# Performance work log

Measured on AMD Instinct MI355X. Metric: run time of the kernel, lower is better.

The kernel has to match this reference:

```python
import jax, jax.numpy as jnp
import numpy as np

B, T, C, H = 2, 2048, 1024, 16
D = C // H  # head dim, even
NEG = -1e10  # masked_fill value used by the torch module (not -inf)


def _rope_cache(dim, max_positions):
    # Faithful to source: theta_i = 1/10000**(-2*(i-1)/dim), i = arange(dim//2)
    i = jnp.arange(dim // 2, dtype=jnp.float32)
    theta = 1.0 / (10000.0 ** (-2.0 * (i - 1.0) / dim))
    ang = jnp.arange(max_positions, dtype=jnp.float32)[:, None] * theta[None, :]  # [T, D/2]
    return jnp.cos(ang), jnp.sin(ang)


def _apply_rope(x, cos, sin):
    # x: [B,H,T,D]; consecutive pairs form complex numbers (x[...,2j], x[...,2j+1])
    xp = x.reshape(*x.shape[:-1], D // 2, 2)
    xr, xi = xp[..., 0], xp[..., 1]
    rr = xr * cos - xi * sin
    ri = xr * sin + xi * cos
    return jnp.stack([rr, ri], axis=-1).reshape(x.shape)


def setup_inputs() -> dict:
    key = jax.random.key(0)
    ks = jax.random.split(key, 5)
    s = 1.0 / np.sqrt(C)
    return {
        'x': jax.random.normal(ks[0], (B, T, C), jnp.float32),
        'Wq': jax.random.normal(ks[1], (C, C), jnp.float32) * s,
        'bq': jnp.zeros((C,), jnp.float32),
        'Wk': jax.random.normal(ks[2], (C, C), jnp.float32) * s,
        'bk': jnp.zeros((C,), jnp.float32),
        'Wv': jax.random.normal(ks[3], (C, C), jnp.float32) * s,
        'bv': jnp.zeros((C,), jnp.float32),
        'Wp': jax.random.normal(ks[4], (C, C), jnp.float32) * s,
        'bp': jnp.zeros((C,), jnp.float32),
    }


def reference(x, Wq, bq, Wk, bk, Wv, bv, Wp, bp):
    cos, sin = _rope_cache(D, T)  # [T, D/2]
    def split_heads(h):
        return h.reshape(B, T, H, D).transpose(0, 2, 1, 3)  # [B,H,T,D]
    q = split_heads(x @ Wq.T + bq)
    k = split_heads(x @ Wk.T + bk)
    v = split_heads(x @ Wv.T + bv)
    q = _apply_rope(q, cos, sin)
    k = _apply_rope(k, cos, sin)
    att = jnp.einsum('bhqd,bhkd->bhqk', q, k) * (1.0 / np.sqrt(D))  # [B,H,T,T]
    causal = jnp.tril(jnp.ones((T, T), bool))
    att = jnp.where(causal, att, NEG)
    att = jax.nn.softmax(att, axis=-1)
    y = jnp.einsum('bhqk,bhkd->bhqd', att, v)
    y = y.transpose(0, 2, 1, 3).reshape(B, T, C)
    return y @ Wp.T + bp
```

## Files before the change

### kernel.cpp

```cpp
#include <hip/hip_runtime.h>

#define SEQ 2048
#define CDIM 1024
#define NHEAD 16
#define HDIM 64

typedef __bf16 bf16x8 __attribute__((ext_vector_type(8)));
typedef __bf16 bf16x4v __attribute__((ext_vector_type(4)));
typedef float f32x4 __attribute__((ext_vector_type(4)));

typedef const __attribute__((address_space(1))) char* gcp_t;
typedef __attribute__((address_space(3))) char* lcp_t;

__device__ __forceinline__ void gload16(const void* g, void* l) {
    __builtin_amdgcn_global_load_lds((gcp_t)g, (lcp_t)l, 16, 0, 0);
}

__device__ __forceinline__ unsigned short f2bf(float f) {
    unsigned int u = __float_as_uint(f);
    u += 0x7fffu + ((u >> 16) & 1u);
    return (unsigned short)(u >> 16);
}

__device__ __forceinline__ int swz16(int r) { return ((r >> 1) & 3) << 4; }


__global__ void cvt_all(const float* __restrict__ x,
                        const float* __restrict__ Wq, const float* __restrict__ Wk,
                        const float* __restrict__ Wv, const float* __restrict__ Wp,
                        unsigned short* __restrict__ xb,
                        unsigned short* __restrict__ wqkv, unsigned short* __restrict__ wpb) {
    int i = blockIdx.x * blockDim.x + threadIdx.x;
    const float* s;
    unsigned short* d;
    int r;
    if (i < 1048576) { s = x; d = xb; r = i; }
    else {
        int j = i - 1048576;
        int which = j >> 18; r = j & 262143;
        s = (which == 0) ? Wq : (which == 1) ? Wk : (which == 2) ? Wv : Wp;
        d = (which < 3) ? (wqkv + (size_t)which * 1048576) : wpb;
    }
    float4 v = ((const float4*)s)[r];
    ushort4 o;
    o.x = f2bf(v.x); o.y = f2bf(v.y); o.z = f2bf(v.z); o.w = f2bf(v.w);
    ((ushort4*)d)[r] = o;
}

__global__ void rope_kernel(float2* __restrict__ cstab) {
    int idx = blockIdx.x * blockDim.x + threadIdx.x;
    int j = idx & 31, t = idx >> 5;
    float e = -2.0f * ((float)j - 1.0f) / 64.0f;
    float denom = (float)pow(10000.0, (double)e);
    float theta = 1.0f / denom;
    float ang = (float)t * theta;
    cstab[idx] = make_float2(cosf(ang), sinf(ang));
}

__global__ __launch_bounds__(512, 1) void gemm_qkv(
    const unsigned short* __restrict__ A, const unsigned short* __restrict__ Bm,
    const float* __restrict__ b0, const float* __restrict__ b1, const float* __restrict__ b2,
    unsigned short* __restrict__ qb, unsigned short* __restrict__ kb,
    unsigned short* __restrict__ vtb, const float2* __restrict__ cstab)
{
    constexpr int NT = 16;
    __shared__ __align__(16) char As[2][256 * 128];
    __shared__ __align__(16) char Bs2[2][192 * 128];
    const int tid = threadIdx.x, lane = tid & 63, wid = tid >> 6;
    const int wr = wid >> 2, wc = wid & 3;
    const int bid = blockIdx.x;
    const int swz = (bid & 7) * 32 + (bid >> 3);
    const int mt = swz >> 4, ntl = swz & 15;
    const int m0 = mt * 256, n0 = ntl * 192;

    f32x4 acc[8][3] = {};

    const char* Ag = (const char*)A + (size_t)m0 * 2048;
    const char* Bg = (const char*)Bm + (size_t)n0 * 2048;
    const int r0 = tid >> 3, cb = (tid & 7) * 16;

    auto stage = [&](int k0, int bufi) {
#pragma unroll
        for (int v = 0; v < 4; ++v) {
            const int r = r0 + 64 * v;
            gload16(Ag + (size_t)r * 2048 + k0 * 2 + (cb ^ ((r & 7) << 4)),
                    As[bufi] + v * 8192 + wid * 1024);
        }
#pragma unroll
        for (int v = 0; v < 3; ++v) {
            const int r = r0 + 64 * v;
            gload16(Bg + (size_t)r * 2048 + k0 * 2 + (cb ^ ((r & 7) << 4)),
                    Bs2[bufi] + v * 8192 + wid * 1024);
        }
    };

    stage(0, 0);
    asm volatile("s_waitcnt vmcnt(0)" ::: "memory");
    __builtin_amdgcn_s_barrier();

    for (int t = 0; t < NT; ++t) {
        const int cur = t & 1;
        if (t + 1 < NT) stage((t + 1) * 64, cur ^ 1);
        const char* Ac = As[cur];
        const char* Bc = Bs2[cur];
#pragma unroll
        for (int kf = 0; kf < 2; ++kf) {
            bf16x8 bfr[3];
#pragma unroll
            for (int fc = 0; fc < 3; ++fc) {
                const int r = wc * 48 + fc * 16 + (lane & 15);
                bfr[fc] = *(const bf16x8*)(Bc + r * 128 + ((kf * 64 + (lane >> 4) * 16) ^ ((r & 7) << 4)));
            }
            __builtin_amdgcn_s_setprio(1);
#pragma unroll
            for (int fr = 0; fr < 8; ++fr) {
                const int r = wr * 128 + fr * 16 + (lane & 15);
                bf16x8 af = *(const bf16x8*)(Ac + r * 128 + ((kf * 64 + (lane >> 4) * 16) ^ ((r & 7) << 4)));
#pragma unroll
                for (int fc = 0; fc < 3; ++fc)
                    acc[fr][fc] = __builtin_amdgcn_mfma_f32_16x16x32_bf16(af, bfr[fc], acc[fr][fc], 0, 0, 0);
            }
            __builtin_amdgcn_s_setprio(0);
        }
        asm volatile("s_waitcnt vmcnt(0)" ::: "memory");
        __builtin_amdgcn_s_barrier();
    }

    const float QSCL = 0.18033688011112042f;
#pragma unroll
    for (int fc = 0; fc < 3; ++fc) {
        const int ng = n0 + wc * 48 + fc * 16 + (lane & 15);
        const int which = ng >> 10, nl = ng & 1023;
        const int h = nl >> 6, d = nl & 63;
        const float* bptr = (which == 0) ? b0 : (which == 1) ? b1 : b2;
        const float bias = bptr[nl];
        if (which < 2) {
            unsigned short* dst = (which == 0) ? qb : kb;
            const float qs = (which == 0) ? QSCL : 1.0f;
            const int j = d >> 1;
#pragma unroll
            for (int fr = 0; fr < 8; ++fr) {
#pragma unroll
                for (int i = 0; i < 4; ++i) {
                    const int row = m0 + wr * 128 + fr * 16 + (lane >> 4) * 4 + i;
                    const int bb = row >> 11, tt = row & 2047;
                    float v = acc[fr][fc][i] + bias;
                    float pp = __shfl_xor(v, 1);
                    const float2 cs = cstab[tt * 32 + j];
                    v = (d & 1) ? fmaf(v, cs.x, pp * cs.y) : fmaf(v, cs.x, -pp * cs.y);
                    dst[((size_t)((bb * 16 + h) * 2048 + tt)) * 64 + d] = f2bf(v * qs);
                }
            }
        } else {
#pragma unroll
            for (int fr = 0; fr < 8; ++fr) {
                const int rowb = m0 + wr * 128 + fr * 16 + (lane >> 4) * 4;
                const int bb = rowb >> 11, tt = rowb & 2047;
                ushort4 pk;
                pk.x = f2bf(acc[fr][fc][0] + bias);
                pk.y = f2bf(acc[fr][fc][1] + bias);
                pk.z = f2bf(acc[fr][fc][2] + bias);
                pk.w = f2bf(acc[fr][fc][3] + bias);
                *(ushort4*)(vtb + ((size_t)((bb * 16 + h) * 64 + d)) * 2048 + tt) = pk;
            }
        }
    }
}

template <int MODE, int BM>
__global__ __launch_bounds__(256) void gemm_bt(
    const unsigned short* __restrict__ A, const unsigned short* __restrict__ Bm,
    const float* __restrict__ b0,
    float* __restrict__ outf)
{
    constexpr int K = 1024;
    constexpr int NIT = K / 32;
    constexpr int NR = (BM == 128) ? 4 : 2;
    __shared__ __align__(16) char As[2][BM * 64];
    __shared__ __align__(16) char Bs[2][128 * 64];
    const int tid = threadIdx.x, lane = tid & 63, wid = tid >> 6;
    const int m0 = blockIdx.y * BM, n0 = blockIdx.x * 128;
    const int wr = (BM == 128) ? ((wid >> 1) * 64) : 0;
    const int wc = (BM == 128) ? ((wid & 1) * 64) : (wid * 32);

    f32x4 acc[4][NR] = {};

    const char* Ag = (const char*)(A + (size_t)m0 * K);
    const char* Bg = (const char*)(Bm + (size_t)n0 * K);
    const int r0 = tid >> 2, cb = (tid & 3) * 16;
    const int ldsw = wid << 10;

    auto stage = [&](int k0, int bufi) {
        char* Ad = As[bufi];
        char* Bd = Bs[bufi];
        gload16(Ag + (size_t)r0 * 2048 + k0 * 2 + (cb ^ swz16(r0)), Ad + ldsw);
        if constexpr (BM == 128)
            gload16(Ag + (size_t)(r0 + 64) * 2048 + k0 * 2 + (cb ^ swz16(r0 + 64)), Ad + 4096 + ldsw);
        gload16(Bg + (size_t)r0 * 2048 + k0 * 2 + (cb ^ swz16(r0)), Bd + ldsw);
        gload16(Bg + (size_t)(r0 + 64) * 2048 + k0 * 2 + (cb ^ swz16(r0 + 64)), Bd + 4096 + ldsw);
    };

    stage(0, 0);
    __syncthreads();

    for (int it = 0; it < NIT; ++it) {
        const int cur = it & 1;
        if (it + 1 < NIT) stage((it + 1) * 32, cur ^ 1);
        const char* Ac = As[cur];
        const char* Bc = Bs[cur];
        const int fs = (lane >> 4) * 16;
        bf16x8 af[4], bfr[NR];
#pragma unroll
        for (int am = 0; am < 4; ++am) {
            const int r = wr + am * 16 + (lane & 15);
            af[am] = *(const bf16x8*)(Ac + r * 64 + (fs ^ swz16(r)));
        }
#pragma unroll
        for (int an = 0; an < NR; ++an) {
            const int r = wc + an * 16 + (lane & 15);
            bfr[an] = *(const bf16x8*)(Bc + r * 64 + (fs ^ swz16(r)));
        }
#pragma unroll
        for (int am = 0; am < 4; ++am)
#pragma unroll
            for (int an = 0; an < NR; ++an)
                acc[am][an] = __builtin_amdgcn_mfma_f32_16x16x32_bf16(af[am], bfr[an], acc[am][an], 0, 0, 0);
        __syncthreads();
    }

#pragma unroll
    for (int an = 0; an < NR; ++an) {
        const int col = n0 + wc + an * 16 + (lane & 15);
        const float bias = b0[col];
#pragma unroll
        for (int am = 0; am < 4; ++am)
#pragma unroll
            for (int i = 0; i < 4; ++i) {
                const int row = m0 + wr + am * 16 + (lane >> 4) * 4 + i;
                outf[(size_t)row * 1024 + col] = acc[am][an][i] + bias;
            }
    }
}

__global__ __launch_bounds__(256) void attn_kernel(
    const unsigned short* __restrict__ qb, const unsigned short* __restrict__ kb,
    const unsigned short* __restrict__ vtb, unsigned short* __restrict__ yb)
{
    __shared__ __align__(16) unsigned short Ks[2][64 * 64];
    __shared__ __align__(16) unsigned short Vs[2][64 * 64];
    __shared__ __align__(16) unsigned short Ps[4][16 * 64];
    const int tid = threadIdx.x, lane = tid & 63, wid = tid >> 6;
    const int bh = blockIdx.y;
    const int b = bh >> 4, h = bh & 15;
    const int qt = (bh & 16) ? (31 - blockIdx.x) : blockIdx.x;
    const int q0 = qt * 64;
    const int qw = q0 + wid * 16;
    const unsigned short* Qg = qb + (size_t)bh * SEQ * HDIM;
    const char* Kg = (const char*)(kb + (size_t)bh * SEQ * HDIM);
    const char* Vg = (const char*)(vtb + (size_t)bh * HDIM * SEQ);

    bf16x8 qf[2];
#pragma unroll
    for (int kf = 0; kf < 2; ++kf)
        qf[kf] = *(const bf16x8*)(Qg + (size_t)(qw + (lane & 15)) * 64 + kf * 32 + (lane >> 4) * 8);

    f32x4 o[4] = {};
    float mrun = -3e38f;
    float lrun = 0.0f;

    const int nt = qt + 1;
    const int cr0 = tid >> 3, cc0 = ((tid & 7) * 16) ^ ((cr0 & 7) << 4);
    const int cr1 = cr0 + 32, cc1 = ((tid & 7) * 16) ^ ((cr1 & 7) << 4);
    const int ldsw = wid << 10;

    auto stage = [&](int kt, int bufi) {
        const size_t kv0 = (size_t)kt * 64;
        gload16(Kg + (kv0 + cr0) * 128 + cc0, (char*)Ks[bufi] + ldsw);
        gload16(Kg + (kv0 + cr1) * 128 + cc1, (char*)Ks[bufi] + 4096 + ldsw);
        gload16(Vg + (size_t)cr0 * 4096 + kv0 * 2 + cc0, (char*)Vs[bufi] + ldsw);
        gload16(Vg + (size_t)cr1 * 4096 + kv0 * 2 + cc1, (char*)Vs[bufi] + 4096 + ldsw);
    };

    stage(0, 0);
    __syncthreads();

    for (int kt = 0; kt < nt; ++kt) {
        const int cur = kt & 1;
        if (kt + 1 < nt) stage(kt + 1, cur ^ 1);
        const int kv0 = kt * 64;
        {
            f32x4 s[4] = {};
            __builtin_amdgcn_s_setprio(1);
#pragma unroll
            for (int kf = 0; kf < 2; ++kf) {
                bf16x8 kfr[4];
#pragma unroll
                for (int an = 0; an < 4; ++an) {
                    const int r = an * 16 + (lane & 15);
                    kfr[an] = *(const bf16x8*)((const char*)Ks[cur] + r * 128 + ((kf * 64 + (lane >> 4) * 16) ^ ((r & 7) << 4)));
                }
#pragma unroll
                for (int an = 0; an < 4; ++an)
                    s[an] = __builtin_amdgcn_mfma_f32_16x16x32_bf16(kfr[an], qf[kf], s[an], 0, 0, 0);
            }
            __builtin_amdgcn_s_setprio(0);
            const bool need_mask = (kv0 + 63 > qw);
            const int qg = qw + (lane & 15);
            const int kbase = kv0 + ((lane >> 4) << 2);
            float p[4][4];
            float mx = -3e38f;
#pragma unroll
            for (int an = 0; an < 4; ++an)
#pragma unroll
                for (int i = 0; i < 4; ++i) {
                    float v = s[an][i];
                    if (need_mask && (kbase + an * 16 + i > qg)) v = -3e38f;
                    p[an][i] = v;
                    mx = fmaxf(mx, v);
                }
            mx = fmaxf(mx, __shfl_xor(mx, 16));
            mx = fmaxf(mx, __shfl_xor(mx, 32));
            if (!__all(mx <= mrun + 8.0f)) {
                const float mnew = fmaxf(mrun, mx);
                const float fsc = __builtin_amdgcn_exp2f(mrun - mnew);
                lrun *= fsc;
#pragma unroll
                for (int dn = 0; dn < 4; ++dn) o[dn] *= fsc;
                mrun = mnew;
            }
            float rs = 0.0f;
#pragma unroll
            for (int an = 0; an < 4; ++an)
#pragma unroll
                for (int i = 0; i < 4; ++i) {
                    p[an][i] = __builtin_amdgcn_exp2f(p[an][i] - mrun);
                    rs += p[an][i];
                }
            rs += __shfl_xor(rs, 16);
            rs += __shfl_xor(rs, 32);
            lrun += rs;
            const int ql = lane & 15;
            char* pbs = (char*)Ps[wid] + ql * 128;
            const int xr = (ql & 7) << 4;
            const int gb = (lane >> 4) << 3;
#pragma unroll
            for (int an = 0; an < 4; ++an) {
                bf16x4v pk;
                pk[0] = (__bf16)p[an][0]; pk[1] = (__bf16)p[an][1];
                pk[2] = (__bf16)p[an][2]; pk[3] = (__bf16)p[an][3];
                *(bf16x4v*)(pbs + ((an * 32 + gb) ^ xr)) = pk;
            }
            __builtin_amdgcn_s_setprio(1);
#pragma unroll
            for (int kf = 0; kf < 2; ++kf) {
                bf16x8 vf[4], pf;
#pragma unroll
                for (int dn = 0; dn < 4; ++dn) {
                    const int r = dn * 16 + (lane & 15);
                    vf[dn] = *(const bf16x8*)((const char*)Vs[cur] + r * 128 + ((kf * 64 + (lane >> 4) * 16) ^ ((r & 7) << 4)));
                }
                {
                    const int qlr = lane & 15;
                    pf = *(const bf16x8*)((const char*)Ps[wid] + qlr * 128 + ((kf * 64 + (lane >> 4) * 16) ^ ((qlr & 7) << 4)));
                }
#pragma unroll
                for (int dn = 0; dn < 4; ++dn)
                    o[dn] = __builtin_amdgcn_mfma_f32_16x16x32_bf16(vf[dn], pf, o[dn], 0, 0, 0);
            }
            __builtin_amdgcn_s_setprio(0);
        }
        __syncthreads();
    }

    {
        const float inv = 1.0f / lrun;
        const int qg = qw + (lane & 15);
        unsigned short* yrow = yb + (size_t)(b * SEQ + qg) * CDIM + h * 64;
#pragma unroll
        for (int dn = 0; dn < 4; ++dn) {
            const int d = dn * 16 + ((lane >> 4) << 2);
            bf16x4v pk;
            pk[0] = (__bf16)(o[dn][0] * inv);
            pk[1] = (__bf16)(o[dn][1] * inv);
            pk[2] = (__bf16)(o[dn][2] * inv);
            pk[3] = (__bf16)(o[dn][3] * inv);
            *(bf16x4v*)(yrow + d) = pk;
        }
    }
}


extern "C" void kernel_launch(void* const* d_in, const int* in_sizes, int n_in,
                              void* d_out, int out_size, void* d_ws, size_t ws_size,
                              hipStream_t stream) {
    (void)in_sizes; (void)n_in; (void)out_size; (void)ws_size;
    const float* x  = (const float*)d_in[0];
    const float* Wq = (const float*)d_in[1];
    const float* bq = (const float*)d_in[2];
    const float* Wk = (const float*)d_in[3];
    const float* bk = (const float*)d_in[4];
    const float* Wv = (const float*)d_in[5];
    const float* bv = (const float*)d_in[6];
    const float* Wp = (const float*)d_in[7];
    const float* bp = (const float*)d_in[8];
    float* out = (float*)d_out;

    char* ws = (char*)d_ws;
    size_t off = 0;
    auto take = [&](size_t bytes) -> char* {
        char* p = ws + off;
        off = (off + bytes + 255) & ~(size_t)255;
        return p;
    };
    float2* cstab = (float2*)take((size_t)SEQ * 32 * 8);
    unsigned short* xb   = (unsigned short*)take((size_t)4096 * 1024 * 2);
    unsigned short* wqkv = (unsigned short*)take((size_t)3 * 1024 * 1024 * 2);
    unsigned short* wpb  = (unsigned short*)take((size_t)1024 * 1024 * 2);
    unsigned short* qbuf = (unsigned short*)take((size_t)32 * SEQ * HDIM * 2);
    unsigned short* kbuf = (unsigned short*)take((size_t)32 * SEQ * HDIM * 2);
    unsigned short* vtb  = (unsigned short*)take((size_t)32 * HDIM * SEQ * 2);
    unsigned short* yb   = (unsigned short*)take((size_t)4096 * 1024 * 2);

    rope_kernel<<<256, 256, 0, stream>>>(cstab);
    cvt_all<<<8192, 256, 0, stream>>>(x, Wq, Wk, Wv, Wp, xb, wqkv, wpb);

    gemm_qkv<<<256, 512, 0, stream>>>(xb, wqkv, bq, bk, bv, qbuf, kbuf, vtb, cstab);
    dim3 g1(32, 32);
    attn_kernel<<<g1, 256, 0, stream>>>(qbuf, kbuf, vtb, yb);
    dim3 g2(8, 64);
    gemm_bt<1, 64><<<g2, 256, 0, stream>>>(yb, wpb, bp, out);
}
```

Before: 130.8 us.

## Split causal attention KV range into balanced chunks and add combine kernel

Attention blocks now cover a chunk of the key range sized so each block processes about eight key tiles, and write unnormalized bf16 partial outputs plus running max/sum. A new combine kernel merges the chunks with log-sum-exp weights and writes the normalized output. This targets load imbalance and tail effects of the causal triangle. It adds workspace traffic, an extra launch, and bf16 rounding of partials.

```diff
diff --git a/kernel.cpp b/kernel.cpp
--- a/kernel.cpp
+++ b/kernel.cpp
@@ -4,6 +4,7 @@
 #define CDIM 1024
 #define NHEAD 16
 #define HDIM 64
+#define NSLOT 80
 
 typedef __bf16 bf16x8 __attribute__((ext_vector_type(8)));
 typedef __bf16 bf16x4v __attribute__((ext_vector_type(4)));
@@ -21,6 +22,9 @@
     u += 0x7fffu + ((u >> 16) & 1u);
     return (unsigned short)(u >> 16);
 }
+
+__device__ __forceinline__ float bflo(unsigned int u) { return __uint_as_float(u << 16); }
+__device__ __forceinline__ float bfhi(unsigned int u) { return __uint_as_float(u & 0xffff0000u); }
 
 __device__ __forceinline__ int swz16(int r) { return ((r >> 1) & 3) << 4; }
 
@@ -244,15 +248,22 @@
 
 __global__ __launch_bounds__(256) void attn_kernel(
     const unsigned short* __restrict__ qb, const unsigned short* __restrict__ kb,
-    const unsigned short* __restrict__ vtb, unsigned short* __restrict__ yb)
+    const unsigned short* __restrict__ vtb, unsigned short* __restrict__ pb,
+    float2* __restrict__ ml)
 {
     __shared__ __align__(16) unsigned short Ks[2][64 * 64];
     __shared__ __align__(16) unsigned short Vs[2][64 * 64];
     __shared__ __align__(16) unsigned short Ps[4][16 * 64];
     const int tid = threadIdx.x, lane = tid & 63, wid = tid >> 6;
-    const int bh = blockIdx.y;
-    const int b = bh >> 4, h = bh & 15;
-    const int qt = (bh & 16) ? (31 - blockIdx.x) : blockIdx.x;
+    const int bh = blockIdx.x;
+    const int y = blockIdx.y;
+    int qt, ck, nc;
+    if (y < 32)      { qt = 31 - (y >> 2); ck = y & 3; nc = 4; }
+    else if (y < 56) { int t2 = y - 32; int k3 = t2 / 3; qt = 23 - k3; ck = t2 - k3 * 3; nc = 3; }
+    else if (y < 72) { int t2 = y - 56; qt = 15 - (t2 >> 1); ck = t2 & 1; nc = 2; }
+    else             { qt = 7 - (y - 72); ck = 0; nc = 1; }
+    const int nt = qt + 1;
+    const int t0 = ck * nt / nc, t1 = (ck + 1) * nt / nc;
     const int q0 = qt * 64;
     const int qw = q0 + wid * 16;
     const unsigned short* Qg = qb + (size_t)bh * SEQ * HDIM;
@@ -268,7 +279,6 @@
     float mrun = -3e38f;
     float lrun = 0.0f;
 
-    const int nt = qt + 1;
     const int cr0 = tid >> 3, cc0 = ((tid & 7) * 16) ^ ((cr0 & 7) << 4);
     const int cr1 = cr0 + 32, cc1 = ((tid & 7) * 16) ^ ((cr1 & 7) << 4);
     const int ldsw = wid << 10;
@@ -281,12 +291,12 @@
         gload16(Vg + (size_t)cr1 * 4096 + kv0 * 2 + cc1, (char*)Vs[bufi] + 4096 + ldsw);
     };
 
-    stage(0, 0);
+    stage(t0, 0);
     __syncthreads();
 
-    for (int kt = 0; kt < nt; ++kt) {
-        const int cur = kt & 1;
-        if (kt + 1 < nt) stage(kt + 1, cur ^ 1);
+    for (int kt = t0; kt < t1; ++kt) {
+        const int cur = (kt - t0) & 1;
+        if (kt + 1 < t1) stage(kt + 1, cur ^ 1);
         const int kv0 = kt * 64;
         {
             f32x4 s[4] = {};
@@ -373,20 +383,80 @@
     }
 
     {
-        const float inv = 1.0f / lrun;
-        const int qg = qw + (lane & 15);
-        unsigned short* yrow = yb + (size_t)(b * SEQ + qg) * CDIM + h * 64;
+        const size_t sbase = (size_t)bh * NSLOT + y;
+        const int qloc = wid * 16 + (lane & 15);
+        unsigned short* prow = pb + (sbase * 64 + qloc) * 64;
 #pragma unroll
         for (int dn = 0; dn < 4; ++dn) {
             const int d = dn * 16 + ((lane >> 4) << 2);
             bf16x4v pk;
-            pk[0] = (__bf16)(o[dn][0] * inv);
-            pk[1] = (__bf16)(o[dn][1] * inv);
-            pk[2] = (__bf16)(o[dn][2] * inv);
-            pk[3] = (__bf16)(o[dn][3] * inv);
-            *(bf16x4v*)(yrow + d) = pk;
-        }
-    }
+            pk[0] = (__bf16)o[dn][0];
+            pk[1] = (__bf16)o[dn][1];
+            pk[2] = (__bf16)o[dn][2];
+            pk[3] = (__bf16)o[dn][3];
+            *(bf16x4v*)(prow + d) = pk;
+        }
+        if ((lane >> 4) == 0) ml[sbase * 64 + qloc] = make_float2(mrun, lrun);
+    }
+}
+
+__global__ __launch_bounds__(256) void combine_kernel(
+    const unsigned short* __restrict__ pb, const float2* __restrict__ ml,
+    unsigned short* __restrict__ yb)
+{
+    const int qt = blockIdx.x, bh = blockIdx.y;
+    const int b = bh >> 4, h = bh & 15;
+    int base, nc;
+    if (qt >= 24)      { base = (31 - qt) * 4;      nc = 4; }
+    else if (qt >= 16) { base = 32 + (23 - qt) * 3; nc = 3; }
+    else if (qt >= 8)  { base = 56 + (15 - qt) * 2; nc = 2; }
+    else               { base = 72 + (7 - qt);      nc = 1; }
+    const int t = threadIdx.x;
+    const int q = t >> 2;
+    const int d0 = (t & 3) * 16;
+    const size_t sbase = (size_t)bh * NSLOT + base;
+
+    float m[4], l[4];
+    float M = -3e38f;
+#pragma unroll
+    for (int c = 0; c < 4; ++c)
+        if (c < nc) {
+            float2 v = ml[(sbase + c) * 64 + q];
+            m[c] = v.x; l[c] = v.y;
+            M = fmaxf(M, v.x);
+        }
+    float L = 0.0f;
+    float w[4];
+#pragma unroll
+    for (int c = 0; c < 4; ++c)
+        if (c < nc) {
+            w[c] = __builtin_amdgcn_exp2f(m[c] - M);
+            L += l[c] * w[c];
+        }
+    const float invL = 1.0f / L;
+
+    float acc[16] = {};
+#pragma unroll
+    for (int c = 0; c < 4; ++c)
+        if (c < nc) {
+            const float wc = w[c] * invL;
+            const uint4* src = (const uint4*)(pb + ((sbase + c) * 64 + q) * 64 + d0);
+            uint4 A = src[0], B = src[1];
+            const unsigned int ua[8] = {A.x, A.y, A.z, A.w, B.x, B.y, B.z, B.w};
+#pragma unroll
+            for (int k = 0; k < 8; ++k) {
+                acc[2 * k]     = fmaf(wc, bflo(ua[k]), acc[2 * k]);
+                acc[2 * k + 1] = fmaf(wc, bfhi(ua[k]), acc[2 * k + 1]);
+            }
+        }
+
+    unsigned int outw[8];
+#pragma unroll
+    for (int k = 0; k < 8; ++k)
+        outw[k] = (unsigned int)f2bf(acc[2 * k]) | ((unsigned int)f2bf(acc[2 * k + 1]) << 16);
+    uint4* dst = (uint4*)(yb + (size_t)(b * SEQ + qt * 64 + q) * CDIM + h * 64 + d0);
+    dst[0] = make_uint4(outw[0], outw[1], outw[2], outw[3]);
+    dst[1] = make_uint4(outw[4], outw[5], outw[6], outw[7]);
 }
 
 
@@ -420,13 +490,17 @@
     unsigned short* kbuf = (unsigned short*)take((size_t)32 * SEQ * HDIM * 2);
     unsigned short* vtb  = (unsigned short*)take((size_t)32 * HDIM * SEQ * 2);
     unsigned short* yb   = (unsigned short*)take((size_t)4096 * 1024 * 2);
+    unsigned short* pbuf = (unsigned short*)take((size_t)32 * NSLOT * 64 * 64 * 2);
+    float2* mlb          = (float2*)take((size_t)32 * NSLOT * 64 * 8);
 
     rope_kernel<<<256, 256, 0, stream>>>(cstab);
     cvt_all<<<8192, 256, 0, stream>>>(x, Wq, Wk, Wv, Wp, xb, wqkv, wpb);
 
     gemm_qkv<<<256, 512, 0, stream>>>(xb, wqkv, bq, bk, bv, qbuf, kbuf, vtb, cstab);
-    dim3 g1(32, 32);
-    attn_kernel<<<g1, 256, 0, stream>>>(qbuf, kbuf, vtb, yb);
+    dim3 g1(32, NSLOT);
+    attn_kernel<<<g1, 256, 0, stream>>>(qbuf, kbuf, vtb, pbuf, mlb);
+    dim3 gc(32, 32);
+    combine_kernel<<<gc, 256, 0, stream>>>(pbuf, mlb, yb);
     dim3 g2(8, 64);
     gemm_bt<1, 64><<<g2, 256, 0, stream>>>(yb, wpb, bp, out);
 }
```

Result: no change. 132.2 us (+1.1%).
